# Kernel optimization log

Hardware: AMD Instinct MI355X
Metric: run time of the kernel (lower is better)

## Reference

```python
import jax, jax.numpy as jnp
import numpy as np

WEIGHT = 1.0  # init arg `weight`; `threshold` is unused in forward
B, N, M, D = 4, 4096, 4096, 3


def setup_inputs() -> dict:
    key = jax.random.key(0)
    k1, k2 = jax.random.split(key)
    coord = jax.random.normal(k1, (B, N, D), dtype=jnp.float32)
    gt = jax.random.normal(k2, (B, M, D), dtype=jnp.float32)
    return {"coord": coord, "gt": gt}


def reference(coord, gt):
    # Faithful to torch: gt/coord are [B, pts, 3]; transpose(2,1) -> [B, 3, pts]
    g = jnp.transpose(gt, (0, 2, 1))     # [B, 3, M]
    c = jnp.transpose(coord, (0, 2, 1))  # [B, 3, N]
    # dis[b, m, n] = sum_d (g[b,d,m] - c[b,d,n])^2  -> [B, M, N]
    dis = jnp.sum((g[:, :, :, None] - c[:, :, None, :]) ** 2, axis=1)
    match_gt = jnp.min(dis, axis=-1)     # [B, M] nearest coord for each gt point
    match_coord = jnp.min(dis, axis=-2)  # [B, N] nearest gt point for each coord
    res = jnp.mean(match_coord) + jnp.mean(match_gt)
    return WEIGHT * res
```

## Files before the change

kernel.cpp:

```cpp
#include <hip/hip_runtime.h>


#define BATCH   4
#define NPTS    4096
#define HELD_PB 256
#define TILES   16
#define CHUNKS  8
#define CHUNK_SZ 512
#define PHASES  8
#define G       8

__global__ __launch_bounds__(256) void chamfer_init(unsigned int* mins, float* out) {
    int i = blockIdx.x * 256 + threadIdx.x;
    if (i < 2 * BATCH * NPTS) mins[i] = 0x7F800000u;
    if (i == 0) out[0] = 0.0f;
}

__global__ __launch_bounds__(256) void chamfer_pass(
    const float* __restrict__ coord, const float* __restrict__ gt,
    unsigned int* __restrict__ mins)
{
    __shared__ float4 sc[CHUNK_SZ];

    int bx = blockIdx.x;
    int pass  = bx >> 9;
    int r     = bx & 511;
    int b     = r >> 7;
    int tile  = (r >> 3) & 15;
    int chunk = r & 7;

    const float* held = pass ? coord : gt;
    const float* strm = pass ? gt : coord;
    unsigned int* out = mins + pass * (BATCH * NPTS) + b * NPTS;

    int tid = threadIdx.x;

    const float* sbase = strm + (size_t)b * NPTS * 3 + (size_t)chunk * CHUNK_SZ * 3;
    for (int p = tid; p < CHUNK_SZ; p += 256) {
        float x = sbase[p * 3 + 0];
        float y = sbase[p * 3 + 1];
        float z = sbase[p * 3 + 2];
        sc[p] = make_float4(-2.f * x, -2.f * y, -2.f * z, x * x + y * y + z * z);
    }

    int hg = tid >> 3;
    int ph = tid & 7;
    const float* hbase = held + (size_t)b * NPTS * 3;
    int hofs = tile * HELD_PB + hg;

    float hx[G], hy[G], hz[G], h2[G], mn[G];
#pragma unroll
    for (int g = 0; g < G; ++g) {
        int h = hofs + g * 32;
        float x = hbase[h * 3 + 0];
        float y = hbase[h * 3 + 1];
        float z = hbase[h * 3 + 2];
        hx[g] = x; hy[g] = y; hz[g] = z;
        h2[g] = x * x + y * y + z * z;
        mn[g] = INFINITY;
    }
    __syncthreads();

#pragma unroll 4
    for (int it = 0; it < CHUNK_SZ / PHASES; ++it) {
        float4 c = sc[it * PHASES + ph];
#pragma unroll
        for (int g = 0; g < G; ++g) {
            float t = h2[g] + c.w;
            t = fmaf(c.x, hx[g], t);
            t = fmaf(c.y, hy[g], t);
            t = fmaf(c.z, hz[g], t);
            mn[g] = fminf(mn[g], t);
        }
    }

#pragma unroll
    for (int g = 0; g < G; ++g) {
        float v = mn[g];
        v = fminf(v, __shfl_xor(v, 1));
        v = fminf(v, __shfl_xor(v, 2));
        v = fminf(v, __shfl_xor(v, 4));
        mn[g] = v;
    }

    if (ph == 0) {
#pragma unroll
        for (int g = 0; g < G; ++g) {
            unsigned int bits = __float_as_uint(fmaxf(mn[g], 0.0f));
            atomicMin(&out[hofs + g * 32], bits);
        }
    }
}

__global__ __launch_bounds__(256) void chamfer_final(
    const unsigned int* __restrict__ mins, float* __restrict__ out)
{
    __shared__ float wsum[4];
    int tid = threadIdx.x;
    int base = blockIdx.x * 2048 + tid;
    float s = 0.f;
#pragma unroll
    for (int k = 0; k < 8; ++k)
        s += __uint_as_float(mins[base + k * 256]);
    for (int off = 32; off > 0; off >>= 1)
        s += __shfl_down(s, off);
    if ((tid & 63) == 0) wsum[tid >> 6] = s;
    __syncthreads();
    if (tid == 0) {
        float t = wsum[0] + wsum[1] + wsum[2] + wsum[3];
        atomicAdd(out, t * (1.0f / 16384.0f));
    }
}

extern "C" void kernel_launch(void* const* d_in, const int* in_sizes, int n_in,
                              void* d_out, int out_size, void* d_ws, size_t ws_size,
                              hipStream_t stream) {
    const float* coord = (const float*)d_in[0];
    const float* gt    = (const float*)d_in[1];
    float* out = (float*)d_out;
    unsigned int* mins = (unsigned int*)d_ws;

    chamfer_init<<<(2 * BATCH * NPTS + 255) / 256, 256, 0, stream>>>(mins, out);
    chamfer_pass<<<2 * BATCH * TILES * CHUNKS, 256, 0, stream>>>(coord, gt, mins);
    chamfer_final<<<16, 256, 0, stream>>>(mins, out);
}
```

Measured before the change: 72.13 us.

## Stream all chunks per block with double-buffered LDS and drop atomic min pass

Each block now holds 64 points and streams the entire opposing cloud through double-buffered, bank-padded shared memory, so every held point's minimum is complete within the block. This removes the init kernel, the global atomicMin scatter and the second read of the mins array; per-block partial sums are reduced by a single-block final kernel. In exchange the grid shrinks from 1024 to 512 blocks, each with a longer serial loop, so on a large GPU occupancy and load balance may suffer.

```diff
diff --git a/kernel.cpp b/kernel.cpp
--- a/kernel.cpp
+++ b/kernel.cpp
@@ -1,114 +1,124 @@
 #include <hip/hip_runtime.h>
 
 
-#define BATCH   4
-#define NPTS    4096
-#define HELD_PB 256
-#define TILES   16
-#define CHUNKS  8
-#define CHUNK_SZ 512
-#define PHASES  8
-#define G       8
+#define BATCH 4
+#define NPTS  4096
+#define TILE  64
+#define CH    512
+#define NCH   8
+#define PHN   32
+#define G     8
+#define CHP   (CH + CH/8)
 
-__global__ __launch_bounds__(256) void chamfer_init(unsigned int* mins, float* out) {
-    int i = blockIdx.x * 256 + threadIdx.x;
-    if (i < 2 * BATCH * NPTS) mins[i] = 0x7F800000u;
-    if (i == 0) out[0] = 0.0f;
-}
+__device__ __forceinline__ int pad_idx(int p) { return p + (p >> 3); }
 
-__global__ __launch_bounds__(256) void chamfer_pass(
+__global__ __launch_bounds__(256, 2) void chamfer_pass(
     const float* __restrict__ coord, const float* __restrict__ gt,
-    unsigned int* __restrict__ mins)
+    float* __restrict__ partials)
 {
-    __shared__ float4 sc[CHUNK_SZ];
+    __shared__ float4 sc[2][CHP];
+    __shared__ float bsum[8];
 
-    int bx = blockIdx.x;
-    int pass  = bx >> 9;
-    int r     = bx & 511;
-    int b     = r >> 7;
-    int tile  = (r >> 3) & 15;
-    int chunk = r & 7;
+    int bx   = blockIdx.x;
+    int pass = bx >> 8;
+    int r    = bx & 255;
+    int b    = r >> 6;
+    int tile = r & 63;
 
-    const float* held = pass ? coord : gt;
-    const float* strm = pass ? gt : coord;
-    unsigned int* out = mins + pass * (BATCH * NPTS) + b * NPTS;
+    const float* hbase = (pass ? coord : gt) + b * NPTS * 3;
+    const float* sbase = (pass ? gt : coord) + b * NPTS * 3;
 
-    int tid = threadIdx.x;
-
-    const float* sbase = strm + (size_t)b * NPTS * 3 + (size_t)chunk * CHUNK_SZ * 3;
-    for (int p = tid; p < CHUNK_SZ; p += 256) {
-        float x = sbase[p * 3 + 0];
-        float y = sbase[p * 3 + 1];
-        float z = sbase[p * 3 + 2];
-        sc[p] = make_float4(-2.f * x, -2.f * y, -2.f * z, x * x + y * y + z * z);
-    }
-
-    int hg = tid >> 3;
-    int ph = tid & 7;
-    const float* hbase = held + (size_t)b * NPTS * 3;
-    int hofs = tile * HELD_PB + hg;
+    int tid   = threadIdx.x;
+    int hg    = tid >> 5;
+    int ph    = tid & 31;
+    int phofs = ph + (ph >> 3);
 
     float hx[G], hy[G], hz[G], h2[G], mn[G];
+    int h0 = tile * TILE + hg * G;
 #pragma unroll
     for (int g = 0; g < G; ++g) {
-        int h = hofs + g * 32;
-        float x = hbase[h * 3 + 0];
-        float y = hbase[h * 3 + 1];
-        float z = hbase[h * 3 + 2];
+        float x = hbase[(h0 + g) * 3 + 0];
+        float y = hbase[(h0 + g) * 3 + 1];
+        float z = hbase[(h0 + g) * 3 + 2];
         hx[g] = x; hy[g] = y; hz[g] = z;
         h2[g] = x * x + y * y + z * z;
         mn[g] = INFINITY;
     }
+
+    {
+        int p = tid * 2;
+        const float* s0 = sbase + p * 3;
+        float x0 = s0[0], y0 = s0[1], z0 = s0[2];
+        float x1 = s0[3], y1 = s0[4], z1 = s0[5];
+        sc[0][pad_idx(p)]     = make_float4(-2.f*x0, -2.f*y0, -2.f*z0, x0*x0 + y0*y0 + z0*z0);
+        sc[0][pad_idx(p + 1)] = make_float4(-2.f*x1, -2.f*y1, -2.f*z1, x1*x1 + y1*y1 + z1*z1);
+    }
     __syncthreads();
 
+    for (int ch = 0; ch < NCH; ++ch) {
+        if (ch + 1 < NCH) {
+            int p = tid * 2;
+            const float* s0 = sbase + ((ch + 1) * CH + p) * 3;
+            float x0 = s0[0], y0 = s0[1], z0 = s0[2];
+            float x1 = s0[3], y1 = s0[4], z1 = s0[5];
+            int nb = (ch + 1) & 1;
+            sc[nb][pad_idx(p)]     = make_float4(-2.f*x0, -2.f*y0, -2.f*z0, x0*x0 + y0*y0 + z0*z0);
+            sc[nb][pad_idx(p + 1)] = make_float4(-2.f*x1, -2.f*y1, -2.f*z1, x1*x1 + y1*y1 + z1*z1);
+        }
+
+        const float4* cur = sc[ch & 1];
 #pragma unroll 4
-    for (int it = 0; it < CHUNK_SZ / PHASES; ++it) {
-        float4 c = sc[it * PHASES + ph];
+        for (int it = 0; it < CH / PHN; ++it) {
+            float4 c = cur[it * (PHN + PHN / 8) + phofs];
 #pragma unroll
-        for (int g = 0; g < G; ++g) {
-            float t = h2[g] + c.w;
-            t = fmaf(c.x, hx[g], t);
-            t = fmaf(c.y, hy[g], t);
-            t = fmaf(c.z, hz[g], t);
-            mn[g] = fminf(mn[g], t);
+            for (int g = 0; g < G; ++g) {
+                float t = h2[g] + c.w;
+                t = fmaf(c.x, hx[g], t);
+                t = fmaf(c.y, hy[g], t);
+                t = fmaf(c.z, hz[g], t);
+                mn[g] = fminf(mn[g], t);
+            }
         }
+        __syncthreads();
     }
 
+    float s = 0.f;
 #pragma unroll
     for (int g = 0; g < G; ++g) {
         float v = mn[g];
+        v = fminf(v, __shfl_xor(v, 16));
+        v = fminf(v, __shfl_xor(v, 8));
+        v = fminf(v, __shfl_xor(v, 4));
+        v = fminf(v, __shfl_xor(v, 2));
         v = fminf(v, __shfl_xor(v, 1));
-        v = fminf(v, __shfl_xor(v, 2));
-        v = fminf(v, __shfl_xor(v, 4));
-        mn[g] = v;
+        s += fmaxf(v, 0.f);
     }
-
-    if (ph == 0) {
+    if (ph == 0) bsum[hg] = s;
+    __syncthreads();
+    if (tid == 0) {
+        float t = 0.f;
 #pragma unroll
-        for (int g = 0; g < G; ++g) {
-            unsigned int bits = __float_as_uint(fmaxf(mn[g], 0.0f));
-            atomicMin(&out[hofs + g * 32], bits);
-        }
+        for (int i = 0; i < 8; ++i) t += bsum[i];
+        partials[bx] = t;
     }
 }
 
-__global__ __launch_bounds__(256) void chamfer_final(
-    const unsigned int* __restrict__ mins, float* __restrict__ out)
+__global__ __launch_bounds__(512) void chamfer_final(
+    const float* __restrict__ partials, float* __restrict__ out)
 {
-    __shared__ float wsum[4];
+    __shared__ float wsum[8];
     int tid = threadIdx.x;
-    int base = blockIdx.x * 2048 + tid;
-    float s = 0.f;
+    float s = partials[tid];
 #pragma unroll
-    for (int k = 0; k < 8; ++k)
-        s += __uint_as_float(mins[base + k * 256]);
     for (int off = 32; off > 0; off >>= 1)
         s += __shfl_down(s, off);
     if ((tid & 63) == 0) wsum[tid >> 6] = s;
     __syncthreads();
     if (tid == 0) {
-        float t = wsum[0] + wsum[1] + wsum[2] + wsum[3];
-        atomicAdd(out, t * (1.0f / 16384.0f));
+        float t = 0.f;
+#pragma unroll
+        for (int i = 0; i < 8; ++i) t += wsum[i];
+        out[0] = t * (1.0f / 16384.0f);
     }
 }
 
@@ -117,10 +127,9 @@
                               hipStream_t stream) {
     const float* coord = (const float*)d_in[0];
     const float* gt    = (const float*)d_in[1];
+    float* partials = (float*)d_ws;
     float* out = (float*)d_out;
-    unsigned int* mins = (unsigned int*)d_ws;
 
-    chamfer_init<<<(2 * BATCH * NPTS + 255) / 256, 256, 0, stream>>>(mins, out);
-    chamfer_pass<<<2 * BATCH * TILES * CHUNKS, 256, 0, stream>>>(coord, gt, mins);
-    chamfer_final<<<16, 256, 0, stream>>>(mins, out);
+    chamfer_pass<<<512, 256, 0, stream>>>(coord, gt, partials);
+    chamfer_final<<<1, 512, 0, stream>>>(partials, out);
 }
```

Measured after the change: 71.87 us. No clear change (-0.4%).
